# Performance work log

Measured on AMD Instinct MI355X. Metric: run time of the kernel, lower is better.

Reference implementation:

```python
import jax, jax.numpy as jnp
import numpy as np

EPS = 1e-8

def setup_inputs() -> dict:
    key = jax.random.key(0)
    k1, k2 = jax.random.split(key)
    B, D, H, W, K = 32, 256, 64, 64, 64
    X = jax.random.normal(k1, (B, D, H, W), dtype=jnp.float32)
    std1 = 1.0 / float(np.sqrt(K * D))
    codewords = jax.random.uniform(k2, (K, D), dtype=jnp.float32, minval=-std1, maxval=std1)
    return {"X": X, "codewords": codewords}

def reference(X, codewords):
    B, D = X.shape[0], X.shape[1]
    # (B, D, H, W) -> (B, N, D)
    Xf = X.reshape(B, D, -1).transpose(0, 2, 1)
    # pairwise cosine similarity: normalize then matmul -> (B, N, K)
    Xn = Xf / jnp.maximum(jnp.linalg.norm(Xf, axis=-1, keepdims=True), EPS)
    Cn = codewords / jnp.maximum(jnp.linalg.norm(codewords, axis=-1, keepdims=True), EPS)
    L = jnp.einsum('bnd,kd->bnk', Xn, Cn)
    A = jax.nn.softmax(L, axis=2)
    # aggregate: E[b,k,d] = sum_n A[b,n,k] * (Xf[b,n,d] - C[k,d])
    # expressed without materializing the (B,N,K,D) residual tensor:
    E = jnp.einsum('bnk,bnd->bkd', A, Xf) - A.sum(axis=1)[:, :, None] * codewords[None, :, :]
    return E
```

## Files before the change

### kernel.cpp

```cpp
#include <hip/hip_runtime.h>
#include <hip/hip_bf16.h>
#include <hip/hip_fp16.h>
#include <math.h>

#define BB 32
#define DD 256
#define NN 4096
#define KK 64
#define EPSV 1e-8f
#define XSTR 264

typedef __attribute__((ext_vector_type(8))) short short8;
typedef __attribute__((ext_vector_type(4))) float f32x4;

__device__ __forceinline__ unsigned int bf16pair(float a, float b) {
    __hip_bfloat162 h = __float22bfloat162_rn(make_float2(a, b));
    return *(unsigned int*)&h;
}
__device__ __forceinline__ unsigned short bf16one(float a) {
    unsigned int ua = __float_as_uint(a);
    ua += 0x7fffu + ((ua >> 16) & 1u);
    return (unsigned short)(ua >> 16);
}
__device__ __forceinline__ unsigned int f16pair(float a, float b) {
    __half2 h = __float22half2_rn(make_float2(a, b));
    return *(unsigned int*)&h;
}

__device__ __forceinline__ void stage_group(int dbase, int n4, const float4* rr,
                                            unsigned short* xnd_s, unsigned short* xdn_s,
                                            f32x4& ssn) {
    float4 r0 = rr[0], r1 = rr[1], r2 = rr[2], r3 = rr[3];
    ssn.x = fmaf(r0.x, r0.x, ssn.x); ssn.x = fmaf(r1.x, r1.x, ssn.x);
    ssn.x = fmaf(r2.x, r2.x, ssn.x); ssn.x = fmaf(r3.x, r3.x, ssn.x);
    ssn.y = fmaf(r0.y, r0.y, ssn.y); ssn.y = fmaf(r1.y, r1.y, ssn.y);
    ssn.y = fmaf(r2.y, r2.y, ssn.y); ssn.y = fmaf(r3.y, r3.y, ssn.y);
    ssn.z = fmaf(r0.z, r0.z, ssn.z); ssn.z = fmaf(r1.z, r1.z, ssn.z);
    ssn.z = fmaf(r2.z, r2.z, ssn.z); ssn.z = fmaf(r3.z, r3.z, ssn.z);
    ssn.w = fmaf(r0.w, r0.w, ssn.w); ssn.w = fmaf(r1.w, r1.w, ssn.w);
    ssn.w = fmaf(r2.w, r2.w, ssn.w); ssn.w = fmaf(r3.w, r3.w, ssn.w);
#pragma unroll
    for (int j = 0; j < 4; j++) {
        int d = dbase + j;
        uint2 u;
        u.x = bf16pair(rr[j].x, rr[j].y);
        u.y = bf16pair(rr[j].z, rr[j].w);
        *(uint2*)(xdn_s + d * 64 + ((((n4 >> 3) ^ (d & 7)) << 3) | (n4 & 7))) = u;
    }
    {
        float col[4][4] = {{r0.x, r1.x, r2.x, r3.x},
                           {r0.y, r1.y, r2.y, r3.y},
                           {r0.z, r1.z, r2.z, r3.z},
                           {r0.w, r1.w, r2.w, r3.w}};
#pragma unroll
        for (int j = 0; j < 4; j++) {
            int n = n4 + j;
            uint2 u;
            u.x = bf16pair(col[j][0], col[j][1]);
            u.y = bf16pair(col[j][2], col[j][3]);
            int blk = (dbase >> 3) ^ ((n >> 2) & 3);
            *(uint2*)(xnd_s + n * XSTR + (blk << 3) + (dbase & 7)) = u;
        }
    }
}

__global__ __launch_bounds__(512, 2) void k_fused(const float* __restrict__ X,
                                                  const float* __restrict__ C,
                                                  __half* __restrict__ P,
                                                  float* __restrict__ Sp) {
    __shared__ unsigned short xnd_s[64 * XSTR];
    __shared__ unsigned short xdn_s[DD * 64];
    __shared__ unsigned short at_s[KK * 72];
    __shared__ float rn4[8 * 64];
    __shared__ float red_s[8 * 64];

    int t = threadIdx.x;
    int b = blockIdx.x >> 4, chunk = blockIdx.x & 15;
    int w = t >> 6, lane = t & 63, c = lane & 15, g = lane >> 4;
    int q2 = t >> 4;
    int n4 = c * 4;
    int kw = w & 3, nh = w >> 2;

    const float* Xb = X + (size_t)b * DD * NN + chunk * 256;

    float4 pre[4];
    {
        const float* xb = Xb + (size_t)(q2 * 4) * NN + n4;
#pragma unroll
        for (int j = 0; j < 4; j++) pre[j] = *(const float4*)(xb + (size_t)j * NN);
    }

    short8 cnf[8];
    {
        int k = 16 * kw + c;
        const float* cp = C + k * DD;
        float4 v0[8], v1[8];
        float ss = 0.f;
#pragma unroll
        for (int ks = 0; ks < 8; ks++) {
            v0[ks] = *(const float4*)(cp + 32 * ks + 8 * g);
            v1[ks] = *(const float4*)(cp + 32 * ks + 8 * g + 4);
            ss = fmaf(v0[ks].x, v0[ks].x, ss); ss = fmaf(v0[ks].y, v0[ks].y, ss);
            ss = fmaf(v0[ks].z, v0[ks].z, ss); ss = fmaf(v0[ks].w, v0[ks].w, ss);
            ss = fmaf(v1[ks].x, v1[ks].x, ss); ss = fmaf(v1[ks].y, v1[ks].y, ss);
            ss = fmaf(v1[ks].z, v1[ks].z, ss); ss = fmaf(v1[ks].w, v1[ks].w, ss);
        }
        ss += __shfl_xor(ss, 16);
        ss += __shfl_xor(ss, 32);
        float r = 1.f / fmaxf(sqrtf(ss), EPSV);
#pragma unroll
        for (int ks = 0; ks < 8; ks++) {
            uint4 u;
            u.x = bf16pair(v0[ks].x * r, v0[ks].y * r);
            u.y = bf16pair(v0[ks].z * r, v0[ks].w * r);
            u.z = bf16pair(v1[ks].x * r, v1[ks].y * r);
            u.w = bf16pair(v1[ks].z * r, v1[ks].w * r);
            cnf[ks] = *(short8*)&u;
        }
    }

    f32x4 eacc[2][4];
#pragma unroll
    for (int dt = 0; dt < 2; dt++)
#pragma unroll
        for (int kt = 0; kt < 4; kt++) eacc[dt][kt] = (f32x4){0.f, 0.f, 0.f, 0.f};
    float s_acc[4] = {0.f, 0.f, 0.f, 0.f};

    for (int p = 0; p < 4; p++) {
        float4 cur[4];
        {
            const float* xb = Xb + (size_t)(q2 * 4 + 128) * NN + p * 64 + n4;
#pragma unroll
            for (int j = 0; j < 4; j++) cur[j] = *(const float4*)(xb + (size_t)j * NN);
        }
        __syncthreads();

        f32x4 ssn = (f32x4){0.f, 0.f, 0.f, 0.f};
        stage_group(q2 * 4, n4, pre, xnd_s, xdn_s, ssn);

        if (p < 3) {
            const float* xb = Xb + (size_t)(q2 * 4) * NN + (p + 1) * 64 + n4;
#pragma unroll
            for (int j = 0; j < 4; j++) pre[j] = *(const float4*)(xb + (size_t)j * NN);
        }

        stage_group(q2 * 4 + 128, n4, cur, xnd_s, xdn_s, ssn);

        ssn.x += __shfl_xor(ssn.x, 16); ssn.x += __shfl_xor(ssn.x, 32);
        ssn.y += __shfl_xor(ssn.y, 16); ssn.y += __shfl_xor(ssn.y, 32);
        ssn.z += __shfl_xor(ssn.z, 16); ssn.z += __shfl_xor(ssn.z, 32);
        ssn.w += __shfl_xor(ssn.w, 16); ssn.w += __shfl_xor(ssn.w, 32);
        if (g == 0) *(f32x4*)(rn4 + w * 64 + n4) = ssn;

        __syncthreads();

        f32x4 lacc[2];
#pragma unroll
        for (int nt = 0; nt < 2; nt++) lacc[nt] = (f32x4){0.f, 0.f, 0.f, 0.f};
#pragma unroll
        for (int ks = 0; ks < 8; ks++) {
            short8 af = cnf[ks];
#pragma unroll
            for (int nt = 0; nt < 2; nt++) {
                int n = 32 * nh + nt * 16 + c;
                short8 bf = *(const short8*)(xnd_s + n * XSTR +
                                             (((4 * ks + g) ^ ((n >> 2) & 3)) << 3));
                lacc[nt] = __builtin_amdgcn_mfma_f32_16x16x32_bf16(af, bf, lacc[nt], 0, 0, 0);
            }
        }

        float lv[2][4];
#pragma unroll
        for (int nt = 0; nt < 2; nt++) {
            int n = 32 * nh + nt * 16 + c;
            float ssq = rn4[n] + rn4[64 + n] + rn4[128 + n] + rn4[192 + n] +
                        rn4[256 + n] + rn4[320 + n] + rn4[384 + n] + rn4[448 + n];
            float rn = 1.f / fmaxf(sqrtf(ssq), EPSV);
            float s = 0.f;
#pragma unroll
            for (int r = 0; r < 4; r++) {
                lv[nt][r] = __expf(lacc[nt][r] * rn);
                s += lv[nt][r];
            }
            s += __shfl_xor(s, 16);
            s += __shfl_xor(s, 32);
            if (g == 0) red_s[w * 64 + n] = s;
        }
        __syncthreads();

#pragma unroll
        for (int nt = 0; nt < 2; nt++) {
            int n = 32 * nh + nt * 16 + c;
            float denom = red_s[(4 * nh + 0) * 64 + n] + red_s[(4 * nh + 1) * 64 + n] +
                          red_s[(4 * nh + 2) * 64 + n] + red_s[(4 * nh + 3) * 64 + n];
            float inv = 1.f / denom;
#pragma unroll
            for (int r = 0; r < 4; r++) {
                float a = lv[nt][r] * inv;
                s_acc[r] += a;
                int k = 16 * kw + 4 * g + r;
                at_s[k * 72 + ((((n >> 3) ^ (k & 7)) << 3) | (n & 7))] = bf16one(a);
            }
        }
        __syncthreads();

#pragma unroll
        for (int ks2 = 0; ks2 < 2; ks2++) {
            short8 bk[4];
#pragma unroll
            for (int kt = 0; kt < 4; kt++) {
                int k = kt * 16 + c;
                bk[kt] = *(const short8*)(at_s + k * 72 + (((4 * ks2 + g) ^ (k & 7)) << 3));
            }
#pragma unroll
            for (int dt = 0; dt < 2; dt++) {
                int d = 32 * w + dt * 16 + c;
                short8 af = *(const short8*)(xdn_s + d * 64 + (((4 * ks2 + g) ^ (d & 7)) << 3));
#pragma unroll
                for (int kt = 0; kt < 4; kt++)
                    eacc[dt][kt] =
                        __builtin_amdgcn_mfma_f32_16x16x32_bf16(af, bk[kt], eacc[dt][kt], 0, 0, 0);
            }
        }
    }

    __half* Pb = P + (size_t)blockIdx.x * (DD * KK);
#pragma unroll
    for (int dt = 0; dt < 2; dt++)
#pragma unroll
        for (int kt = 0; kt < 4; kt++) {
            int k = kt * 16 + c;
            int d0 = 32 * w + dt * 16 + 4 * g;
            f32x4 e = eacc[dt][kt];
            uint2 u;
            u.x = f16pair(e.x, e.y);
            u.y = f16pair(e.z, e.w);
            *(uint2*)(Pb + (size_t)k * DD + d0) = u;
        }

#pragma unroll
    for (int r = 0; r < 4; r++) {
        float v = s_acc[r];
        v += __shfl_xor(v, 1);
        v += __shfl_xor(v, 2);
        v += __shfl_xor(v, 4);
        v += __shfl_xor(v, 8);
        if (c == 0) red_s[w * 64 + 16 * kw + 4 * g + r] = v;
    }
    __syncthreads();
    if (t < KK) {
        int k = t;
        int kw2 = k >> 4;
        Sp[blockIdx.x * 64 + k] = red_s[kw2 * 64 + k] + red_s[(kw2 + 4) * 64 + k];
    }
}

__global__ __launch_bounds__(256) void k_fin(const __half* __restrict__ P,
                                             const float* __restrict__ Sp,
                                             const float* __restrict__ C,
                                             float* __restrict__ out) {
    int idx = blockIdx.x * 256 + threadIdx.x;
    int b = idx >> 12;
    int r = idx & 4095;
    int k = r >> 6;
    int d0 = (r & 63) * 4;
    const __half* Pp = P + (size_t)b * 16 * (DD * KK) + k * DD + d0;
    const float* Sb = Sp + b * 16 * 64 + k;
    f32x4 e0 = (f32x4){0.f, 0.f, 0.f, 0.f};
    f32x4 e1 = (f32x4){0.f, 0.f, 0.f, 0.f};
    float s0 = 0.f, s1 = 0.f;
#pragma unroll
    for (int cc = 0; cc < 16; cc += 2) {
        uint2 v0 = *(const uint2*)(Pp + (size_t)cc * (DD * KK));
        uint2 v1 = *(const uint2*)(Pp + (size_t)(cc + 1) * (DD * KK));
        __half2 a0 = *(__half2*)&v0.x, a1 = *(__half2*)&v0.y;
        __half2 b0 = *(__half2*)&v1.x, b1 = *(__half2*)&v1.y;
        e0.x += __low2float(a0); e0.y += __high2float(a0);
        e0.z += __low2float(a1); e0.w += __high2float(a1);
        e1.x += __low2float(b0); e1.y += __high2float(b0);
        e1.z += __low2float(b1); e1.w += __high2float(b1);
        s0 += Sb[cc * 64];
        s1 += Sb[(cc + 1) * 64];
    }
    f32x4 cv = *(const f32x4*)(C + k * DD + d0);
    f32x4 e = e0 + e1;
    float s = s0 + s1;
    f32x4 o;
    o.x = e.x - s * cv.x;
    o.y = e.y - s * cv.y;
    o.z = e.z - s * cv.z;
    o.w = e.w - s * cv.w;
    *(f32x4*)(out + (size_t)(b * 64 + k) * DD + d0) = o;
}

extern "C" void kernel_launch(void* const* d_in, const int* in_sizes, int n_in,
                              void* d_out, int out_size, void* d_ws, size_t ws_size,
                              hipStream_t stream) {
    const float* X = (const float*)d_in[0];
    const float* C = (const float*)d_in[1];
    float* out = (float*)d_out;
    unsigned char* ws = (unsigned char*)d_ws;

    float* Sp = (float*)ws;
    __half* P = (__half*)(ws + 131072);

    k_fused<<<512, 512, 0, stream>>>(X, C, P, Sp);
    k_fin<<<512, 256, 0, stream>>>(P, Sp, C, out);
}
```

Measured before the change: 211.5 us.

## Double-buffer xnd tile in LDS and feed E-MFMA operands directly from global

Removes the transposed xdn LDS copy. The second MFMA stage now loads X rows straight from global memory (likely L2 hits) and converts them to bf16 in registers. The xnd tile is double-buffered so the next chunk is staged during the current softmax, which drops one barrier per iteration. This trades LDS writes, LDS footprint and synchronisation for extra global reloads of X, and the reworked barrier order carries some risk of a race on rn4.

```diff
diff --git a/kernel.cpp b/kernel.cpp
--- a/kernel.cpp
+++ b/kernel.cpp
@@ -27,9 +27,8 @@
     return *(unsigned int*)&h;
 }
 
-__device__ __forceinline__ void stage_group(int dbase, int n4, const float4* rr,
-                                            unsigned short* xnd_s, unsigned short* xdn_s,
-                                            f32x4& ssn) {
+__device__ __forceinline__ void stage_xnd(int dbase, int n4, const float4* rr,
+                                          unsigned short* xnd, f32x4& ssn) {
     float4 r0 = rr[0], r1 = rr[1], r2 = rr[2], r3 = rr[3];
     ssn.x = fmaf(r0.x, r0.x, ssn.x); ssn.x = fmaf(r1.x, r1.x, ssn.x);
     ssn.x = fmaf(r2.x, r2.x, ssn.x); ssn.x = fmaf(r3.x, r3.x, ssn.x);
@@ -39,28 +38,18 @@
     ssn.z = fmaf(r2.z, r2.z, ssn.z); ssn.z = fmaf(r3.z, r3.z, ssn.z);
     ssn.w = fmaf(r0.w, r0.w, ssn.w); ssn.w = fmaf(r1.w, r1.w, ssn.w);
     ssn.w = fmaf(r2.w, r2.w, ssn.w); ssn.w = fmaf(r3.w, r3.w, ssn.w);
+    float col[4][4] = {{r0.x, r1.x, r2.x, r3.x},
+                       {r0.y, r1.y, r2.y, r3.y},
+                       {r0.z, r1.z, r2.z, r3.z},
+                       {r0.w, r1.w, r2.w, r3.w}};
 #pragma unroll
     for (int j = 0; j < 4; j++) {
-        int d = dbase + j;
+        int n = n4 + j;
         uint2 u;
-        u.x = bf16pair(rr[j].x, rr[j].y);
-        u.y = bf16pair(rr[j].z, rr[j].w);
-        *(uint2*)(xdn_s + d * 64 + ((((n4 >> 3) ^ (d & 7)) << 3) | (n4 & 7))) = u;
-    }
-    {
-        float col[4][4] = {{r0.x, r1.x, r2.x, r3.x},
-                           {r0.y, r1.y, r2.y, r3.y},
-                           {r0.z, r1.z, r2.z, r3.z},
-                           {r0.w, r1.w, r2.w, r3.w}};
-#pragma unroll
-        for (int j = 0; j < 4; j++) {
-            int n = n4 + j;
-            uint2 u;
-            u.x = bf16pair(col[j][0], col[j][1]);
-            u.y = bf16pair(col[j][2], col[j][3]);
-            int blk = (dbase >> 3) ^ ((n >> 2) & 3);
-            *(uint2*)(xnd_s + n * XSTR + (blk << 3) + (dbase & 7)) = u;
-        }
+        u.x = bf16pair(col[j][0], col[j][1]);
+        u.y = bf16pair(col[j][2], col[j][3]);
+        int blk = (dbase >> 3) ^ ((n >> 2) & 3);
+        *(uint2*)(xnd + n * XSTR + (blk << 3) + (dbase & 7)) = u;
     }
 }
 
@@ -68,9 +57,8 @@
                                                   const float* __restrict__ C,
                                                   __half* __restrict__ P,
                                                   float* __restrict__ Sp) {
-    __shared__ unsigned short xnd_s[64 * XSTR];
-    __shared__ unsigned short xdn_s[DD * 64];
-    __shared__ unsigned short at_s[KK * 72];
+    __shared__ unsigned short xnd_s[2 * 64 * XSTR];
+    __shared__ unsigned short at_s[KK * 64];
     __shared__ float rn4[8 * 64];
     __shared__ float red_s[8 * 64];
 
@@ -82,13 +70,6 @@
     int kw = w & 3, nh = w >> 2;
 
     const float* Xb = X + (size_t)b * DD * NN + chunk * 256;
-
-    float4 pre[4];
-    {
-        const float* xb = Xb + (size_t)(q2 * 4) * NN + n4;
-#pragma unroll
-        for (int j = 0; j < 4; j++) pre[j] = *(const float4*)(xb + (size_t)j * NN);
-    }
 
     short8 cnf[8];
     {
@@ -119,6 +100,32 @@
         }
     }
 
+    float4 ld[4];
+    {
+        const float* xb = Xb + (size_t)(q2 * 4) * NN + n4;
+#pragma unroll
+        for (int j = 0; j < 4; j++) ld[j] = *(const float4*)(xb + (size_t)j * NN);
+    }
+    {
+        f32x4 ssn0 = (f32x4){0.f, 0.f, 0.f, 0.f};
+        stage_xnd(q2 * 4, n4, ld, xnd_s, ssn0);
+        const float* xb = Xb + (size_t)(q2 * 4 + 128) * NN + n4;
+#pragma unroll
+        for (int j = 0; j < 4; j++) ld[j] = *(const float4*)(xb + (size_t)j * NN);
+        stage_xnd(q2 * 4 + 128, n4, ld, xnd_s, ssn0);
+        ssn0.x += __shfl_xor(ssn0.x, 16); ssn0.x += __shfl_xor(ssn0.x, 32);
+        ssn0.y += __shfl_xor(ssn0.y, 16); ssn0.y += __shfl_xor(ssn0.y, 32);
+        ssn0.z += __shfl_xor(ssn0.z, 16); ssn0.z += __shfl_xor(ssn0.z, 32);
+        ssn0.w += __shfl_xor(ssn0.w, 16); ssn0.w += __shfl_xor(ssn0.w, 32);
+        if (g == 0) *(f32x4*)(rn4 + w * 64 + n4) = ssn0;
+    }
+    {
+        const float* xb = Xb + (size_t)(q2 * 4) * NN + 64 + n4;
+#pragma unroll
+        for (int j = 0; j < 4; j++) ld[j] = *(const float4*)(xb + (size_t)j * NN);
+    }
+    __syncthreads();
+
     f32x4 eacc[2][4];
 #pragma unroll
     for (int dt = 0; dt < 2; dt++)
@@ -127,32 +134,16 @@
     float s_acc[4] = {0.f, 0.f, 0.f, 0.f};
 
     for (int p = 0; p < 4; p++) {
-        float4 cur[4];
-        {
-            const float* xb = Xb + (size_t)(q2 * 4 + 128) * NN + p * 64 + n4;
-#pragma unroll
-            for (int j = 0; j < 4; j++) cur[j] = *(const float4*)(xb + (size_t)j * NN);
-        }
-        __syncthreads();
+        unsigned short* xc = xnd_s + (p & 1) * (64 * XSTR);
+        unsigned short* xn = xnd_s + ((p & 1) ^ 1) * (64 * XSTR);
 
         f32x4 ssn = (f32x4){0.f, 0.f, 0.f, 0.f};
-        stage_group(q2 * 4, n4, pre, xnd_s, xdn_s, ssn);
-
         if (p < 3) {
-            const float* xb = Xb + (size_t)(q2 * 4) * NN + (p + 1) * 64 + n4;
-#pragma unroll
-            for (int j = 0; j < 4; j++) pre[j] = *(const float4*)(xb + (size_t)j * NN);
-        }
-
-        stage_group(q2 * 4 + 128, n4, cur, xnd_s, xdn_s, ssn);
-
-        ssn.x += __shfl_xor(ssn.x, 16); ssn.x += __shfl_xor(ssn.x, 32);
-        ssn.y += __shfl_xor(ssn.y, 16); ssn.y += __shfl_xor(ssn.y, 32);
-        ssn.z += __shfl_xor(ssn.z, 16); ssn.z += __shfl_xor(ssn.z, 32);
-        ssn.w += __shfl_xor(ssn.w, 16); ssn.w += __shfl_xor(ssn.w, 32);
-        if (g == 0) *(f32x4*)(rn4 + w * 64 + n4) = ssn;
-
-        __syncthreads();
+            stage_xnd(q2 * 4, n4, ld, xn, ssn);
+            const float* xb = Xb + (size_t)(q2 * 4 + 128) * NN + (p + 1) * 64 + n4;
+#pragma unroll
+            for (int j = 0; j < 4; j++) ld[j] = *(const float4*)(xb + (size_t)j * NN);
+        }
 
         f32x4 lacc[2];
 #pragma unroll
@@ -163,7 +154,7 @@
 #pragma unroll
             for (int nt = 0; nt < 2; nt++) {
                 int n = 32 * nh + nt * 16 + c;
-                short8 bf = *(const short8*)(xnd_s + n * XSTR +
+                short8 bf = *(const short8*)(xc + n * XSTR +
                                              (((4 * ks + g) ^ ((n >> 2) & 3)) << 3));
                 lacc[nt] = __builtin_amdgcn_mfma_f32_16x16x32_bf16(af, bf, lacc[nt], 0, 0, 0);
             }
@@ -199,28 +190,80 @@
                 float a = lv[nt][r] * inv;
                 s_acc[r] += a;
                 int k = 16 * kw + 4 * g + r;
-                at_s[k * 72 + ((((n >> 3) ^ (k & 7)) << 3) | (n & 7))] = bf16one(a);
+                at_s[k * 64 + ((((n >> 3) ^ (k & 7)) << 3) | (n & 7))] = bf16one(a);
             }
         }
+
+        if (p < 3) {
+            stage_xnd(q2 * 4 + 128, n4, ld, xn, ssn);
+            ssn.x += __shfl_xor(ssn.x, 16); ssn.x += __shfl_xor(ssn.x, 32);
+            ssn.y += __shfl_xor(ssn.y, 16); ssn.y += __shfl_xor(ssn.y, 32);
+            ssn.z += __shfl_xor(ssn.z, 16); ssn.z += __shfl_xor(ssn.z, 32);
+            ssn.w += __shfl_xor(ssn.w, 16); ssn.w += __shfl_xor(ssn.w, 32);
+            if (g == 0) *(f32x4*)(rn4 + w * 64 + n4) = ssn;
+            if (p < 2) {
+                const float* xb = Xb + (size_t)(q2 * 4) * NN + (p + 2) * 64 + n4;
+#pragma unroll
+                for (int j = 0; j < 4; j++) ld[j] = *(const float4*)(xb + (size_t)j * NN);
+            }
+        }
+
+        float4 ax[4];
+#pragma unroll
+        for (int dt = 0; dt < 2; dt++) {
+            const float* xa = Xb + (size_t)(32 * w + dt * 16 + c) * NN + p * 64 + 8 * g;
+            ax[2 * dt + 0] = *(const float4*)(xa);
+            ax[2 * dt + 1] = *(const float4*)(xa + 4);
+        }
         __syncthreads();
 
-#pragma unroll
-        for (int ks2 = 0; ks2 < 2; ks2++) {
-            short8 bk[4];
-#pragma unroll
-            for (int kt = 0; kt < 4; kt++) {
-                int k = kt * 16 + c;
-                bk[kt] = *(const short8*)(at_s + k * 72 + (((4 * ks2 + g) ^ (k & 7)) << 3));
-            }
-#pragma unroll
-            for (int dt = 0; dt < 2; dt++) {
-                int d = 32 * w + dt * 16 + c;
-                short8 af = *(const short8*)(xdn_s + d * 64 + (((4 * ks2 + g) ^ (d & 7)) << 3));
-#pragma unroll
-                for (int kt = 0; kt < 4; kt++)
-                    eacc[dt][kt] =
-                        __builtin_amdgcn_mfma_f32_16x16x32_bf16(af, bk[kt], eacc[dt][kt], 0, 0, 0);
-            }
+        short8 bk[4];
+#pragma unroll
+        for (int kt = 0; kt < 4; kt++) {
+            int k = kt * 16 + c;
+            bk[kt] = *(const short8*)(at_s + k * 64 + (((0 + g) ^ (k & 7)) << 3));
+        }
+        short8 af0[2];
+#pragma unroll
+        for (int dt = 0; dt < 2; dt++) {
+            float4 f0 = ax[2 * dt + 0], f1 = ax[2 * dt + 1];
+            uint4 u;
+            u.x = bf16pair(f0.x, f0.y);
+            u.y = bf16pair(f0.z, f0.w);
+            u.z = bf16pair(f1.x, f1.y);
+            u.w = bf16pair(f1.z, f1.w);
+            af0[dt] = *(short8*)&u;
+        }
+#pragma unroll
+        for (int dt = 0; dt < 2; dt++) {
+            const float* xa = Xb + (size_t)(32 * w + dt * 16 + c) * NN + p * 64 + 32 + 8 * g;
+            ax[2 * dt + 0] = *(const float4*)(xa);
+            ax[2 * dt + 1] = *(const float4*)(xa + 4);
+        }
+#pragma unroll
+        for (int dt = 0; dt < 2; dt++)
+#pragma unroll
+            for (int kt = 0; kt < 4; kt++)
+                eacc[dt][kt] =
+                    __builtin_amdgcn_mfma_f32_16x16x32_bf16(af0[dt], bk[kt], eacc[dt][kt], 0, 0, 0);
+#pragma unroll
+        for (int kt = 0; kt < 4; kt++) {
+            int k = kt * 16 + c;
+            bk[kt] = *(const short8*)(at_s + k * 64 + (((4 + g) ^ (k & 7)) << 3));
+        }
+#pragma unroll
+        for (int dt = 0; dt < 2; dt++) {
+            float4 f0 = ax[2 * dt + 0], f1 = ax[2 * dt + 1];
+            uint4 u;
+            u.x = bf16pair(f0.x, f0.y);
+            u.y = bf16pair(f0.z, f0.w);
+            u.z = bf16pair(f1.x, f1.y);
+            u.w = bf16pair(f1.z, f1.w);
+            short8 af1 = *(short8*)&u;
+#pragma unroll
+            for (int kt = 0; kt < 4; kt++)
+                eacc[dt][kt] =
+                    __builtin_amdgcn_mfma_f32_16x16x32_bf16(af1, bk[kt], eacc[dt][kt], 0, 0, 0);
         }
     }
 
```

After: 213.9 us. No clear change (+1.1%).
